# Performance work log

Measured on AMD Instinct MI355X. Metric: run time of the kernel, lower is better.

## Reference

```python
import jax, jax.numpy as jnp
import numpy as np

B, T, E, H = 2, 1024, 1024, 16
D = E // H  # per-head dim = 64; softmax scale uses sqrt(D) per SelfAttentionHead.embedding_dim
SCALE = float(np.sqrt(D))


def setup_inputs() -> dict:
    key = jax.random.key(0)
    ks = jax.random.split(key, 10)
    s = 1.0 / np.sqrt(D)
    sf = 1.0 / np.sqrt(E)
    return {
        "x": jax.random.normal(ks[0], (B, T, E), dtype=jnp.float32),
        # per-head linear params, stacked over head index i: (H, D, D) / (H, D)
        "Wq": jax.random.uniform(ks[1], (H, D, D), minval=-s, maxval=s, dtype=jnp.float32),
        "bq": jax.random.uniform(ks[2], (H, D), minval=-s, maxval=s, dtype=jnp.float32),
        "Wk": jax.random.uniform(ks[3], (H, D, D), minval=-s, maxval=s, dtype=jnp.float32),
        "bk": jax.random.uniform(ks[4], (H, D), minval=-s, maxval=s, dtype=jnp.float32),
        "Wv": jax.random.uniform(ks[5], (H, D, D), minval=-s, maxval=s, dtype=jnp.float32),
        "bv": jax.random.uniform(ks[6], (H, D), minval=-s, maxval=s, dtype=jnp.float32),
        "Wf": jax.random.uniform(ks[7], (E, E), minval=-sf, maxval=sf, dtype=jnp.float32),
        "bf": jax.random.uniform(ks[8], (E,), minval=-sf, maxval=sf, dtype=jnp.float32),
    }


def reference(x, Wq, bq, Wk, bk, Wv, bv, Wf, bf):
    # (B, T, E) -> (B, H, T, D)
    xh = x.reshape(B, T, H, D).transpose(0, 2, 1, 3)
    # each head i applies its own D->D linears to the FULL (B,H,T,D) tensor
    # q/k/v: (B, H, T, I, D) where I indexes the head (param set)
    q = jnp.einsum('bhtd,ied->bhtie', xh, Wq) + bq
    k = jnp.einsum('bhtd,ied->bhtie', xh, Wk) + bk
    v = jnp.einsum('bhtd,ied->bhtie', xh, Wv) + bv
    # attention over the FEATURE dimension: scores are (B,H,I,D,D)
    scores = jnp.einsum('bhtip,bhtiq->bhipq', q, k) / SCALE
    w = jax.nn.softmax(scores, axis=-1)
    # (B,H,I,D,D) x (B,H,T,I,D) -> (B,H,T,I,D)
    o = jnp.einsum('bhipq,bhtiq->bhtip', w, v)
    # concat head outputs along last dim: (B,H,T,I*D) = (B,H,T,E)
    cat = o.reshape(B, H, T, E)
    # final Linear(E,E)
    return jnp.einsum('bhte,fe->bhtf', cat, Wf) + bf
```

## Files before the change

### kernel.cpp

```cpp
#include <hip/hip_runtime.h>

#define BB 2
#define TT 1024
#define EE 1024
#define HH 16
#define DD 64

typedef __attribute__((ext_vector_type(8))) short short8;
typedef __attribute__((ext_vector_type(4))) float floatx4;
typedef __attribute__((ext_vector_type(4))) unsigned short ushort4v;
typedef __attribute__((ext_vector_type(8))) unsigned short ushort8v;

static __device__ __forceinline__ unsigned short f2bf(float f) {
  union { float f; unsigned int u; } v; v.f = f;
  unsigned int u = v.u;
  u += 0x7FFFu + ((u >> 16) & 1u);
  return (unsigned short)(u >> 16);
}
static __device__ __forceinline__ float bf2f(unsigned short u) {
  union { unsigned int i; float f; } v; v.i = ((unsigned int)u) << 16;
  return v.f;
}
static __device__ __forceinline__ void splitbf(float x, unsigned short& h,
                                               unsigned short& l) {
  h = f2bf(x);
  l = f2bf(x - bf2f(h));
}
static __device__ __forceinline__ unsigned short* lp(const unsigned short* t,
                                                     int row, int byte) {
  return (unsigned short*)((const char*)t + row * 128 + (byte ^ ((row & 7) << 4)));
}
static __device__ __forceinline__ short8 ldf(const unsigned short* t, int row,
                                             int byte) {
  return *(const short8*)((const char*)t + row * 128 + (byte ^ ((row & 7) << 4)));
}

__global__ __launch_bounds__(256) void kP(const float* __restrict__ x,
                                          const float* __restrict__ Wf,
                                          float* __restrict__ Sxx_part,
                                          float* __restrict__ sx_part,
                                          unsigned short* __restrict__ Wfbf,
                                          unsigned short* __restrict__ xbf) {
  const int bx = blockIdx.x;
  const int r = threadIdx.x;
  if (bx >= 256) {
    const int wb = bx - 256;
#pragma unroll
    for (int it = 0; it < 4; ++it) {
      int idx = wb * 4096 + it * 1024 + r * 4;
      float4 v = *reinterpret_cast<const float4*>(&Wf[idx]);
      ushort4v o;
      o[0] = f2bf(v.x); o[1] = f2bf(v.y); o[2] = f2bf(v.z); o[3] = f2bf(v.w);
      *reinterpret_cast<ushort4v*>(&Wfbf[idx]) = o;
    }
    return;
  }
  const int bh = bx >> 3, chunk = bx & 7;
  const int b = bh >> 4, h = bh & 15;
  const int t0 = chunk * 128;
  __shared__ float Xs[128 * 64];
  const float* xb = x + ((size_t)b * TT + t0) * EE + h * 64;
#pragma unroll
  for (int j = 0; j < 8; ++j) {
    int idx4 = j * 256 + r;
    int t = idx4 >> 4, c4 = idx4 & 15;
    *reinterpret_cast<float4*>(&Xs[t * 64 + c4 * 4]) =
        *reinterpret_cast<const float4*>(&xb[(size_t)t * EE + c4 * 4]);
  }
  __syncthreads();
#pragma unroll
  for (int j = 0; j < 4; ++j) {
    int idx8 = j * 256 + r;
    int t = idx8 >> 3, gch = idx8 & 7;
    ushort8v o;
#pragma unroll
    for (int e = 0; e < 8; ++e) o[e] = f2bf(Xs[t * 64 + gch * 8 + e]);
    *reinterpret_cast<ushort8v*>(&xbf[((size_t)bh * TT + t0 + t) * 64 + gch * 8]) = o;
  }
  const int p0 = (r >> 4) * 4, q0 = (r & 15) * 4;
  float acc[4][4] = {};
  for (int t = 0; t < 128; ++t) {
    float4 pv = *reinterpret_cast<const float4*>(&Xs[t * 64 + p0]);
    float4 qv = *reinterpret_cast<const float4*>(&Xs[t * 64 + q0]);
    float pa[4] = {pv.x, pv.y, pv.z, pv.w};
    float qa[4] = {qv.x, qv.y, qv.z, qv.w};
#pragma unroll
    for (int i = 0; i < 4; ++i)
#pragma unroll
      for (int j = 0; j < 4; ++j) acc[i][j] += pa[i] * qa[j];
  }
  float* Sb = Sxx_part + ((size_t)chunk * 32 + bh) * 4096;
#pragma unroll
  for (int i = 0; i < 4; ++i) {
    float4 v = make_float4(acc[i][0], acc[i][1], acc[i][2], acc[i][3]);
    *reinterpret_cast<float4*>(&Sb[(p0 + i) * 64 + q0]) = v;
  }
  if (r < 64) {
    float s = 0.f;
    for (int t = 0; t < 128; ++t) s += Xs[t * 64 + r];
    sx_part[(chunk * 32 + bh) * 64 + r] = s;
  }
}

__global__ __launch_bounds__(256) void kB1(const float* __restrict__ Sxx_part,
                                           const float* __restrict__ sx_part,
                                           const float* __restrict__ Wq,
                                           const float* __restrict__ bq,
                                           const float* __restrict__ Wk,
                                           const float* __restrict__ bk,
                                           const float* __restrict__ Wv,
                                           const float* __restrict__ bv,
                                           unsigned short* __restrict__ Mtbf) {
  const int blk = blockIdx.x;
  const int bh = blk >> 4, ih = blk & 15;
  const int r = threadIdx.x;
  const int w = r >> 6, l = r & 63;
  const int wm = w >> 1, wn = w & 1;
  const int lm = l & 15, lk = l >> 4;

  __shared__ unsigned short TSh[4096], TSl[4096];
  __shared__ unsigned short TWh[4096], TWl[4096];
  __shared__ unsigned short TAh[4096], TAl[4096];
  __shared__ float SC[64 * 68];
  __shared__ float svec[64], qsv[64], ksv[64], bqv[64], bkv[64], bvv[64];

#pragma unroll
  for (int it = 0; it < 4; ++it) {
    int idx = it * 1024 + r * 4;
    int row = idx >> 6, c0 = idx & 63;
    float4 vs = *(const float4*)&Sxx_part[(size_t)bh * 4096 + idx];
#pragma unroll
    for (int ch = 1; ch < 8; ++ch) {
      float4 tv = *(const float4*)&Sxx_part[((size_t)ch * 32 + bh) * 4096 + idx];
      vs.x += tv.x; vs.y += tv.y; vs.z += tv.z; vs.w += tv.w;
    }
    float4 vw = *(const float4*)&Wq[ih * 4096 + idx];
    float fs[4] = {vs.x, vs.y, vs.z, vs.w};
    float fw[4] = {vw.x, vw.y, vw.z, vw.w};
    ushort4v sh, sl, wh, wl;
#pragma unroll
    for (int j = 0; j < 4; ++j) {
      unsigned short th, tl;
      splitbf(fs[j], th, tl);
      sh[j] = th; sl[j] = tl;
      splitbf(fw[j], th, tl);
      wh[j] = th; wl[j] = tl;
    }
    *(ushort4v*)lp(TSh, row, c0 * 2) = sh;
    *(ushort4v*)lp(TSl, row, c0 * 2) = sl;
    *(ushort4v*)lp(TWh, row, c0 * 2) = wh;
    *(ushort4v*)lp(TWl, row, c0 * 2) = wl;
  }
  if (r < 64) {
    float s = 0.f;
#pragma unroll
    for (int ch = 0; ch < 8; ++ch) s += sx_part[(ch * 32 + bh) * 64 + r];
    svec[r] = s;
    bqv[r] = bq[ih * 64 + r];
    bkv[r] = bk[ih * 64 + r];
    bvv[r] = bv[ih * 64 + r];
  }
  __syncthreads();

  floatx4 a1[2][2] = {};
  {
    short8 Ah[2][2], Al[2][2], Bh[2][2], Bl[2][2];
#pragma unroll
    for (int mt = 0; mt < 2; ++mt)
#pragma unroll
      for (int ks = 0; ks < 2; ++ks) {
        Ah[mt][ks] = ldf(TWh, wm * 32 + mt * 16 + lm, ks * 64 + lk * 16);
        Al[mt][ks] = ldf(TWl, wm * 32 + mt * 16 + lm, ks * 64 + lk * 16);
        Bh[mt][ks] = ldf(TSh, wn * 32 + mt * 16 + lm, ks * 64 + lk * 16);
        Bl[mt][ks] = ldf(TSl, wn * 32 + mt * 16 + lm, ks * 64 + lk * 16);
      }
#pragma unroll
    for (int ks = 0; ks < 2; ++ks)
#pragma unroll
      for (int mt = 0; mt < 2; ++mt)
#pragma unroll
        for (int nt = 0; nt < 2; ++nt) {
          a1[mt][nt] = __builtin_amdgcn_mfma_f32_16x16x32_bf16(Ah[mt][ks], Bh[nt][ks], a1[mt][nt], 0, 0, 0);
          a1[mt][nt] = __builtin_amdgcn_mfma_f32_16x16x32_bf16(Ah[mt][ks], Bl[nt][ks], a1[mt][nt], 0, 0, 0);
          a1[mt][nt] = __builtin_amdgcn_mfma_f32_16x16x32_bf16(Al[mt][ks], Bh[nt][ks], a1[mt][nt], 0, 0, 0);
        }
  }
#pragma unroll
  for (int mt = 0; mt < 2; ++mt)
#pragma unroll
    for (int nt = 0; nt < 2; ++nt)
#pragma unroll
      for (int q = 0; q < 4; ++q) {
        int p = wm * 32 + mt * 16 + lk * 4 + q;
        int dd = wn * 32 + nt * 16 + lm;
        unsigned short h, lo2;
        splitbf(a1[mt][nt][q], h, lo2);
        *lp(TAh, p, dd * 2) = h;
        *lp(TAl, p, dd * 2) = lo2;
      }
  {
    int p = r >> 2, dc = (r & 3) * 16;
    float s = 0.f;
#pragma unroll
    for (int j = 0; j < 16; ++j) {
      int d = dc + j;
      s += (bf2f(*lp(TWh, p, d * 2)) + bf2f(*lp(TWl, p, d * 2))) * svec[d];
    }
    s += __shfl_xor(s, 1);
    s += __shfl_xor(s, 2);
    if ((r & 3) == 0) qsv[p] = s;
  }
  __syncthreads();

#pragma unroll
  for (int it = 0; it < 4; ++it) {
    int idx = it * 1024 + r * 4;
    int row = idx >> 6, c0 = idx & 63;
    float4 vw = *(const float4*)&Wk[ih * 4096 + idx];
    float fw[4] = {vw.x, vw.y, vw.z, vw.w};
    ushort4v wh, wl;
#pragma unroll
    for (int j = 0; j < 4; ++j) {
      unsigned short th, tl;
      splitbf(fw[j], th, tl);
      wh[j] = th; wl[j] = tl;
    }
    *(ushort4v*)lp(TWh, row, c0 * 2) = wh;
    *(ushort4v*)lp(TWl, row, c0 * 2) = wl;
    float4 vv = *(const float4*)&Wv[ih * 4096 + idx];
    int q = row, d0 = c0;
    *lp(TSh, d0 + 0, q * 2) = f2bf(vv.x);
    *lp(TSh, d0 + 1, q * 2) = f2bf(vv.y);
    *lp(TSh, d0 + 2, q * 2) = f2bf(vv.z);
    *lp(TSh, d0 + 3, q * 2) = f2bf(vv.w);
  }
  __syncthreads();
  {
    int p = r >> 2, dc = (r & 3) * 16;
    float s = 0.f;
#pragma unroll
    for (int j = 0; j < 16; ++j) {
      int d = dc + j;
      s += (bf2f(*lp(TWh, p, d * 2)) + bf2f(*lp(TWl, p, d * 2))) * svec[d];
    }
    s += __shfl_xor(s, 1);
    s += __shfl_xor(s, 2);
    if ((r & 3) == 0) ksv[p] = s;
  }
  floatx4 a2[2][2] = {};
  {
    short8 Ah[2][2], Al[2][2], Bh[2][2], Bl[2][2];
#pragma unroll
    for (int mt = 0; mt < 2; ++mt)
#pragma unroll
      for (int ks = 0; ks < 2; ++ks) {
        Ah[mt][ks] = ldf(TAh, wm * 32 + mt * 16 + lm, ks * 64 + lk * 16);
        Al[mt][ks] = ldf(TAl, wm * 32 + mt * 16 + lm, ks * 64 + lk * 16);
        Bh[mt][ks] = ldf(TWh, wn * 32 + mt * 16 + lm, ks * 64 + lk * 16);
        Bl[mt][ks] = ldf(TWl, wn * 32 + mt * 16 + lm, ks * 64 + lk * 16);
      }
#pragma unroll
    for (int ks = 0; ks < 2; ++ks)
#pragma unroll
      for (int mt = 0; mt < 2; ++mt)
#pragma unroll
        for (int nt = 0; nt < 2; ++nt) {
          a2[mt][nt] = __builtin_amdgcn_mfma_f32_16x16x32_bf16(Ah[mt][ks], Bh[nt][ks], a2[mt][nt], 0, 0, 0);
          a2[mt][nt] = __builtin_amdgcn_mfma_f32_16x16x32_bf16(Ah[mt][ks], Bl[nt][ks], a2[mt][nt], 0, 0, 0);
          a2[mt][nt] = __builtin_amdgcn_mfma_f32_16x16x32_bf16(Al[mt][ks], Bh[nt][ks], a2[mt][nt], 0, 0, 0);
        }
  }
  __syncthreads();
#pragma unroll
  for (int mt = 0; mt < 2; ++mt)
#pragma unroll
    for (int nt = 0; nt < 2; ++nt)
#pragma unroll
      for (int q = 0; q < 4; ++q) {
        int p = wm * 32 + mt * 16 + lk * 4 + q;
        int qq = wn * 32 + nt * 16 + lm;
        float v = a2[mt][nt][q] + qsv[p] * bkv[qq] + bqv[p] * ksv[qq] +
                  1024.f * bqv[p] * bkv[qq];
        SC[p * 68 + qq] = v * 0.125f;
      }
  __syncthreads();
  {
    int p = r >> 2, qc = (r & 3) * 16;
    float e[16];
    float m = -1e30f;
#pragma unroll
    for (int j = 0; j < 16; ++j) {
      e[j] = SC[p * 68 + qc + j];
      m = fmaxf(m, e[j]);
    }
    m = fmaxf(m, __shfl_xor(m, 1));
    m = fmaxf(m, __shfl_xor(m, 2));
    float s = 0.f, cp = 0.f;
#pragma unroll
    for (int j = 0; j < 16; ++j) {
      float ex = __expf(e[j] - m);
      e[j] = ex;
      s += ex;
      cp += ex * bvv[qc + j];
    }
    s += __shfl_xor(s, 1);
    s += __shfl_xor(s, 2);
    cp += __shfl_xor(cp, 1);
    cp += __shfl_xor(cp, 2);
    float inv = 1.f / s;
#pragma unroll
    for (int j = 0; j < 16; ++j) *lp(TSl, p, (qc + j) * 2) = f2bf(e[j] * inv);
    if ((r & 3) == 0)
      Mtbf[(size_t)(2048 + bh) * 1024 + ih * 64 + p] = f2bf(cp * inv);
  }
  __syncthreads();
  floatx4 a3[2][2] = {};
  {
    short8 A3[2][2], B3[2][2];
#pragma unroll
    for (int mt = 0; mt < 2; ++mt)
#pragma unroll
      for (int ks = 0; ks < 2; ++ks) {
        A3[mt][ks] = ldf(TSh, wm * 32 + mt * 16 + lm, ks * 64 + lk * 16);
        B3[mt][ks] = ldf(TSl, wn * 32 + mt * 16 + lm, ks * 64 + lk * 16);
      }
#pragma unroll
    for (int ks = 0; ks < 2; ++ks)
#pragma unroll
      for (int mt = 0; mt < 2; ++mt)
#pragma unroll
        for (int nt = 0; nt < 2; ++nt)
          a3[mt][nt] = __builtin_amdgcn_mfma_f32_16x16x32_bf16(A3[mt][ks], B3[nt][ks], a3[mt][nt], 0, 0, 0);
  }
#pragma unroll
  for (int mt = 0; mt < 2; ++mt)
#pragma unroll
    for (int nt = 0; nt < 2; ++nt)
#pragma unroll
      for (int q = 0; q < 4; ++q) {
        int d = wm * 32 + mt * 16 + lk * 4 + q;
        int p = wn * 32 + nt * 16 + lm;
        Mtbf[(size_t)(bh * 64 + d) * 1024 + ih * 64 + p] = f2bf(a3[mt][nt][q]);
      }
}

__global__ __launch_bounds__(256) void kB2(const unsigned short* __restrict__ Wfbf,
                                           const unsigned short* __restrict__ Mtbf,
                                           const float* __restrict__ bfv,
                                           unsigned short* __restrict__ Gbf,
                                           float* __restrict__ g) {
  const int fx = blockIdx.x, ny = blockIdx.y;
  const int r = threadIdx.x;
  const int w = r >> 6, l = r & 63;
  const int wr = w >> 1, wc = w & 1;
  if (ny == 32 && wc == 1) return;
  const int lm = l & 15, lk = l >> 4;
  const int f_base = fx * 64 + wr * 32;
  const int n_base = ny * 64 + wc * 32;
  const unsigned short* ap = Wfbf + (size_t)(f_base + lm) * 1024 + lk * 8;
  const unsigned short* bp = Mtbf + (size_t)(n_base + lm) * 1024 + lk * 8;
  floatx4 acc[2][2] = {};
  for (int k0 = 0; k0 < 1024; k0 += 64) {
    short8 a[2][2], b[2][2];
#pragma unroll
    for (int mi = 0; mi < 2; ++mi)
#pragma unroll
      for (int ks = 0; ks < 2; ++ks)
        a[mi][ks] = *reinterpret_cast<const short8*>(ap + mi * 16 * 1024 + k0 + ks * 32);
#pragma unroll
    for (int ni = 0; ni < 2; ++ni)
#pragma unroll
      for (int ks = 0; ks < 2; ++ks)
        b[ni][ks] = *reinterpret_cast<const short8*>(bp + ni * 16 * 1024 + k0 + ks * 32);
#pragma unroll
    for (int ks = 0; ks < 2; ++ks)
#pragma unroll
      for (int mi = 0; mi < 2; ++mi)
#pragma unroll
        for (int ni = 0; ni < 2; ++ni)
          acc[mi][ni] = __builtin_amdgcn_mfma_f32_16x16x32_bf16(
              a[mi][ks], b[ni][ks], acc[mi][ni], 0, 0, 0);
  }
  if (ny < 32) {
    const int bh = ny;
#pragma unroll
    for (int mi = 0; mi < 2; ++mi)
#pragma unroll
      for (int ni = 0; ni < 2; ++ni) {
        const int d = wc * 32 + ni * 16 + lm;
        const int fr = f_base + mi * 16 + lk * 4;
#pragma unroll
        for (int q = 0; q < 4; ++q)
          Gbf[(size_t)bh * 65536 + (size_t)(fr + q) * 64 + d] = f2bf(acc[mi][ni][q]);
      }
  } else {
#pragma unroll
    for (int mi = 0; mi < 2; ++mi)
#pragma unroll
      for (int ni = 0; ni < 2; ++ni) {
        const int bh = ni * 16 + lm;
        const int fr = f_base + mi * 16 + lk * 4;
#pragma unroll
        for (int q = 0; q < 4; ++q)
          g[bh * 1024 + fr + q] = acc[mi][ni][q] + bfv[fr + q];
      }
  }
}

__global__ __launch_bounds__(256) void kC(const unsigned short* __restrict__ xbf,
                                          const unsigned short* __restrict__ Gbf,
                                          const float* __restrict__ g,
                                          float* __restrict__ out) {
  const int bh = blockIdx.y;
  const int t0 = (blockIdx.x >> 3) * 128, f0 = (blockIdx.x & 7) * 128;
  const int r = threadIdx.x;
  const int w = r >> 6, l = r & 63;
  const int wr = w >> 1, wc = w & 1;
  const int lm = l & 15, lk = l >> 4;
  const unsigned short* ap =
      xbf + (size_t)bh * 65536 + (size_t)(t0 + wr * 64 + lm) * 64 + lk * 8;
  const unsigned short* bp =
      Gbf + (size_t)bh * 65536 + (size_t)(f0 + wc * 64 + lm) * 64 + lk * 8;
  short8 a[4][2], b[4][2];
#pragma unroll
  for (int mi = 0; mi < 4; ++mi)
#pragma unroll
    for (int ks = 0; ks < 2; ++ks)
      a[mi][ks] = *reinterpret_cast<const short8*>(ap + mi * 16 * 64 + ks * 32);
#pragma unroll
  for (int ni = 0; ni < 4; ++ni)
#pragma unroll
    for (int ks = 0; ks < 2; ++ks)
      b[ni][ks] = *reinterpret_cast<const short8*>(bp + ni * 16 * 64 + ks * 32);
  floatx4 acc[4][4] = {};
#pragma unroll
  for (int ks = 0; ks < 2; ++ks)
#pragma unroll
    for (int mi = 0; mi < 4; ++mi)
#pragma unroll
      for (int ni = 0; ni < 4; ++ni)
        acc[mi][ni] = __builtin_amdgcn_mfma_f32_16x16x32_bf16(
            a[mi][ks], b[ni][ks], acc[mi][ni], 0, 0, 0);
  float gv[4];
#pragma unroll
  for (int ni = 0; ni < 4; ++ni)
    gv[ni] = g[bh * 1024 + f0 + wc * 64 + ni * 16 + lm];
  float* ob = out + (size_t)bh * 1048576;
#pragma unroll
  for (int mi = 0; mi < 4; ++mi)
#pragma unroll
    for (int ni = 0; ni < 4; ++ni) {
      const int f = f0 + wc * 64 + ni * 16 + lm;
#pragma unroll
      for (int q = 0; q < 4; ++q) {
        const int t = t0 + wr * 64 + mi * 16 + lk * 4 + q;
        ob[(size_t)t * 1024 + f] = acc[mi][ni][q] + gv[ni];
      }
    }
}

extern "C" void kernel_launch(void* const* d_in, const int* in_sizes, int n_in,
                              void* d_out, int out_size, void* d_ws, size_t ws_size,
                              hipStream_t stream) {
  const float* x = (const float*)d_in[0];
  const float* Wq = (const float*)d_in[1];
  const float* bq = (const float*)d_in[2];
  const float* Wk = (const float*)d_in[3];
  const float* bk = (const float*)d_in[4];
  const float* Wv = (const float*)d_in[5];
  const float* bv = (const float*)d_in[6];
  const float* Wf = (const float*)d_in[7];
  const float* bf = (const float*)d_in[8];
  float* out = (float*)d_out;

  float* ws = (float*)d_ws;
  float* Sxx_part = ws;
  float* sx_part = Sxx_part + 1048576;
  float* g = sx_part + 16384;
  unsigned short* Wfbf = (unsigned short*)(g + 32768);
  unsigned short* xbf = Wfbf + 1048576;
  unsigned short* Mtbf = xbf + 2097152;
  unsigned short* Gbf = Mtbf + 2162688;

  kP<<<512, 256, 0, stream>>>(x, Wf, Sxx_part, sx_part, Wfbf, xbf);
  kB1<<<512, 256, 0, stream>>>(Sxx_part, sx_part, Wq, bq, Wk, bk, Wv, bv, Mtbf);
  kB2<<<dim3(16, 33), 256, 0, stream>>>(Wfbf, Mtbf, bf, Gbf, g);
  kC<<<dim3(64, 32), 256, 0, stream>>>(xbf, Gbf, g, out);
}
```

Measured before the change: 99.58 us.

## Fuse G=Wf·M product into output kernel via shared-memory staging

Merges the kB2 kernel, which computed the per-head Wf·M product and bias vector g, into the final output kernel. Each block now computes its 128x64 slice of G plus the g row in registers, stages them in LDS, then loops over all T tiles to write the output. This removes a launch and the global round trip for Gbf and g. The cost is redundant-free but coarser parallelism: the grid shrinks from 2048 to 256 blocks, each doing a serial loop over T, which may underuse the GPU.

```diff
diff --git a/kernel.cpp b/kernel.cpp
--- a/kernel.cpp
+++ b/kernel.cpp
@@ -1,10 +1,7 @@
 #include <hip/hip_runtime.h>
 
-#define BB 2
 #define TT 1024
 #define EE 1024
-#define HH 16
-#define DD 64
 
 typedef __attribute__((ext_vector_type(8))) short short8;
 typedef __attribute__((ext_vector_type(4))) float floatx4;
@@ -344,119 +341,123 @@
       }
 }
 
-__global__ __launch_bounds__(256) void kB2(const unsigned short* __restrict__ Wfbf,
-                                           const unsigned short* __restrict__ Mtbf,
-                                           const float* __restrict__ bfv,
-                                           unsigned short* __restrict__ Gbf,
-                                           float* __restrict__ g) {
-  const int fx = blockIdx.x, ny = blockIdx.y;
+__global__ __launch_bounds__(256) void kC(const unsigned short* __restrict__ xbf,
+                                          const unsigned short* __restrict__ Wfbf,
+                                          const unsigned short* __restrict__ Mtbf,
+                                          const float* __restrict__ bfv,
+                                          float* __restrict__ out) {
+  const int fx = blockIdx.x, bh = blockIdx.y;
+  const int f0 = fx * 128;
   const int r = threadIdx.x;
   const int w = r >> 6, l = r & 63;
-  const int wr = w >> 1, wc = w & 1;
-  if (ny == 32 && wc == 1) return;
   const int lm = l & 15, lk = l >> 4;
-  const int f_base = fx * 64 + wr * 32;
-  const int n_base = ny * 64 + wc * 32;
-  const unsigned short* ap = Wfbf + (size_t)(f_base + lm) * 1024 + lk * 8;
-  const unsigned short* bp = Mtbf + (size_t)(n_base + lm) * 1024 + lk * 8;
-  floatx4 acc[2][2] = {};
-  for (int k0 = 0; k0 < 1024; k0 += 64) {
-    short8 a[2][2], b[2][2];
-#pragma unroll
-    for (int mi = 0; mi < 2; ++mi)
+
+  __shared__ __align__(16) unsigned short GT[128 * 64];
+  __shared__ __align__(16) unsigned short cL[1024];
+  __shared__ float gL[128];
+
+  if (r < 128)
+    *reinterpret_cast<ushort8v*>(&cL[r * 8]) = *reinterpret_cast<const ushort8v*>(
+        &Mtbf[(size_t)(2048 + bh) * 1024 + r * 8]);
+  __syncthreads();
+
+  {
+    const int wf = w >> 1, wd = w & 1;
+    const unsigned short* ap = Wfbf + (size_t)(f0 + wf * 64 + lm) * 1024 + lk * 8;
+    const unsigned short* bp = Mtbf + (size_t)(bh * 64 + wd * 32 + lm) * 1024 + lk * 8;
+    floatx4 acc[4][2] = {};
+    floatx4 gacc[4] = {};
+    for (int k0 = 0; k0 < 1024; k0 += 64) {
+      short8 a[4][2], b[2][2], cf[2];
+#pragma unroll
+      for (int mi = 0; mi < 4; ++mi)
+#pragma unroll
+        for (int ks = 0; ks < 2; ++ks)
+          a[mi][ks] = *reinterpret_cast<const short8*>(ap + mi * 16 * 1024 + k0 + ks * 32);
+#pragma unroll
+      for (int ni = 0; ni < 2; ++ni)
+#pragma unroll
+        for (int ks = 0; ks < 2; ++ks)
+          b[ni][ks] = *reinterpret_cast<const short8*>(bp + ni * 16 * 1024 + k0 + ks * 32);
 #pragma unroll
       for (int ks = 0; ks < 2; ++ks)
-        a[mi][ks] = *reinterpret_cast<const short8*>(ap + mi * 16 * 1024 + k0 + ks * 32);
-#pragma unroll
-    for (int ni = 0; ni < 2; ++ni)
+        cf[ks] = *reinterpret_cast<const short8*>(&cL[k0 + ks * 32 + lk * 8]);
 #pragma unroll
       for (int ks = 0; ks < 2; ++ks)
-        b[ni][ks] = *reinterpret_cast<const short8*>(bp + ni * 16 * 1024 + k0 + ks * 32);
+#pragma unroll
+        for (int mi = 0; mi < 4; ++mi) {
+#pragma unroll
+          for (int ni = 0; ni < 2; ++ni)
+            acc[mi][ni] = __builtin_amdgcn_mfma_f32_16x16x32_bf16(
+                a[mi][ks], b[ni][ks], acc[mi][ni], 0, 0, 0);
+          if (wd == 0)
+            gacc[mi] = __builtin_amdgcn_mfma_f32_16x16x32_bf16(
+                a[mi][ks], cf[ks], gacc[mi], 0, 0, 0);
+        }
+    }
+#pragma unroll
+    for (int mi = 0; mi < 4; ++mi)
+#pragma unroll
+      for (int ni = 0; ni < 2; ++ni)
+#pragma unroll
+        for (int q = 0; q < 4; ++q) {
+          int fl = wf * 64 + mi * 16 + lk * 4 + q;
+          int d = wd * 32 + ni * 16 + lm;
+          *lp(GT, fl, d * 2) = f2bf(acc[mi][ni][q]);
+        }
+    if (wd == 0 && lm == 0) {
+#pragma unroll
+      for (int mi = 0; mi < 4; ++mi)
+#pragma unroll
+        for (int q = 0; q < 4; ++q) {
+          int fl = wf * 64 + mi * 16 + lk * 4 + q;
+          gL[fl] = gacc[mi][q] + bfv[f0 + fl];
+        }
+    }
+  }
+  __syncthreads();
+
+  const int wt = w >> 1, wc = w & 1;
+  float gv[4];
+#pragma unroll
+  for (int ni = 0; ni < 4; ++ni) gv[ni] = gL[wc * 64 + ni * 16 + lm];
+  short8 bfr[4][2];
+#pragma unroll
+  for (int ni = 0; ni < 4; ++ni)
 #pragma unroll
     for (int ks = 0; ks < 2; ++ks)
-#pragma unroll
-      for (int mi = 0; mi < 2; ++mi)
-#pragma unroll
-        for (int ni = 0; ni < 2; ++ni)
+      bfr[ni][ks] = ldf(GT, wc * 64 + ni * 16 + lm, (ks * 32 + lk * 8) * 2);
+  float* ob = out + (size_t)bh * 1048576;
+  for (int t0 = 0; t0 < 1024; t0 += 128) {
+    const unsigned short* ap =
+        xbf + (size_t)bh * 65536 + (size_t)(t0 + wt * 64 + lm) * 64 + lk * 8;
+    short8 a[4][2];
+#pragma unroll
+    for (int mi = 0; mi < 4; ++mi)
+#pragma unroll
+      for (int ks = 0; ks < 2; ++ks)
+        a[mi][ks] = *reinterpret_cast<const short8*>(ap + mi * 16 * 64 + ks * 32);
+    floatx4 acc[4][4] = {};
+#pragma unroll
+    for (int ks = 0; ks < 2; ++ks)
+#pragma unroll
+      for (int mi = 0; mi < 4; ++mi)
+#pragma unroll
+        for (int ni = 0; ni < 4; ++ni)
           acc[mi][ni] = __builtin_amdgcn_mfma_f32_16x16x32_bf16(
-              a[mi][ks], b[ni][ks], acc[mi][ni], 0, 0, 0);
-  }
-  if (ny < 32) {
-    const int bh = ny;
-#pragma unroll
-    for (int mi = 0; mi < 2; ++mi)
-#pragma unroll
-      for (int ni = 0; ni < 2; ++ni) {
-        const int d = wc * 32 + ni * 16 + lm;
-        const int fr = f_base + mi * 16 + lk * 4;
-#pragma unroll
-        for (int q = 0; q < 4; ++q)
-          Gbf[(size_t)bh * 65536 + (size_t)(fr + q) * 64 + d] = f2bf(acc[mi][ni][q]);
-      }
-  } else {
-#pragma unroll
-    for (int mi = 0; mi < 2; ++mi)
-#pragma unroll
-      for (int ni = 0; ni < 2; ++ni) {
-        const int bh = ni * 16 + lm;
-        const int fr = f_base + mi * 16 + lk * 4;
-#pragma unroll
-        for (int q = 0; q < 4; ++q)
-          g[bh * 1024 + fr + q] = acc[mi][ni][q] + bfv[fr + q];
-      }
-  }
-}
-
-__global__ __launch_bounds__(256) void kC(const unsigned short* __restrict__ xbf,
-                                          const unsigned short* __restrict__ Gbf,
-                                          const float* __restrict__ g,
-                                          float* __restrict__ out) {
-  const int bh = blockIdx.y;
-  const int t0 = (blockIdx.x >> 3) * 128, f0 = (blockIdx.x & 7) * 128;
-  const int r = threadIdx.x;
-  const int w = r >> 6, l = r & 63;
-  const int wr = w >> 1, wc = w & 1;
-  const int lm = l & 15, lk = l >> 4;
-  const unsigned short* ap =
-      xbf + (size_t)bh * 65536 + (size_t)(t0 + wr * 64 + lm) * 64 + lk * 8;
-  const unsigned short* bp =
-      Gbf + (size_t)bh * 65536 + (size_t)(f0 + wc * 64 + lm) * 64 + lk * 8;
-  short8 a[4][2], b[4][2];
-#pragma unroll
-  for (int mi = 0; mi < 4; ++mi)
-#pragma unroll
-    for (int ks = 0; ks < 2; ++ks)
-      a[mi][ks] = *reinterpret_cast<const short8*>(ap + mi * 16 * 64 + ks * 32);
-#pragma unroll
-  for (int ni = 0; ni < 4; ++ni)
-#pragma unroll
-    for (int ks = 0; ks < 2; ++ks)
-      b[ni][ks] = *reinterpret_cast<const short8*>(bp + ni * 16 * 64 + ks * 32);
-  floatx4 acc[4][4] = {};
-#pragma unroll
-  for (int ks = 0; ks < 2; ++ks)
+              a[mi][ks], bfr[ni][ks], acc[mi][ni], 0, 0, 0);
 #pragma unroll
     for (int mi = 0; mi < 4; ++mi)
 #pragma unroll
-      for (int ni = 0; ni < 4; ++ni)
-        acc[mi][ni] = __builtin_amdgcn_mfma_f32_16x16x32_bf16(
-            a[mi][ks], b[ni][ks], acc[mi][ni], 0, 0, 0);
-  float gv[4];
-#pragma unroll
-  for (int ni = 0; ni < 4; ++ni)
-    gv[ni] = g[bh * 1024 + f0 + wc * 64 + ni * 16 + lm];
-  float* ob = out + (size_t)bh * 1048576;
-#pragma unroll
-  for (int mi = 0; mi < 4; ++mi)
-#pragma unroll
-    for (int ni = 0; ni < 4; ++ni) {
-      const int f = f0 + wc * 64 + ni * 16 + lm;
-#pragma unroll
-      for (int q = 0; q < 4; ++q) {
-        const int t = t0 + wr * 64 + mi * 16 + lk * 4 + q;
-        ob[(size_t)t * 1024 + f] = acc[mi][ni][q] + gv[ni];
-      }
-    }
+      for (int ni = 0; ni < 4; ++ni) {
+        const int f = f0 + wc * 64 + ni * 16 + lm;
+#pragma unroll
+        for (int q = 0; q < 4; ++q) {
+          const int t = t0 + wt * 64 + mi * 16 + lk * 4 + q;
+          ob[(size_t)t * 1024 + f] = acc[mi][ni][q] + gv[ni];
+        }
+      }
+  }
 }
 
 extern "C" void kernel_launch(void* const* d_in, const int* in_sizes, int n_in,
@@ -476,14 +477,11 @@
   float* ws = (float*)d_ws;
   float* Sxx_part = ws;
   float* sx_part = Sxx_part + 1048576;
-  float* g = sx_part + 16384;
-  unsigned short* Wfbf = (unsigned short*)(g + 32768);
+  unsigned short* Wfbf = (unsigned short*)(sx_part + 16384);
   unsigned short* xbf = Wfbf + 1048576;
   unsigned short* Mtbf = xbf + 2097152;
-  unsigned short* Gbf = Mtbf + 2162688;
 
   kP<<<512, 256, 0, stream>>>(x, Wf, Sxx_part, sx_part, Wfbf, xbf);
   kB1<<<512, 256, 0, stream>>>(Sxx_part, sx_part, Wq, bq, Wk, bk, Wv, bv, Mtbf);
-  kB2<<<dim3(16, 33), 256, 0, stream>>>(Wfbf, Mtbf, bf, Gbf, g);
-  kC<<<dim3(64, 32), 256, 0, stream>>>(xbf, Gbf, g, out);
-}
+  kC<<<dim3(8, 32), 256, 0, stream>>>(xbf, Wfbf, Mtbf, bf, out);
+}
```

Result: faster. 82.25 us (-17.4%).
